# Kernel tuning notes

Measured on AMD Instinct MI355X. Metric: run time of the kernel, lower is better.

## Reference

```python
import jax, jax.numpy as jnp
import numpy as np

N, D, H, C = 100000, 128, 8, 16  # nodes, units=H*C, heads, per-head channels
E = 400000                        # edges per edge set (2 edge sets)
LN_EPS = 1e-3                     # keras LayerNormalization default epsilon


def setup_inputs() -> dict:
    key = jax.random.key(0)
    ks = jax.random.split(key, 16)
    def dense(k, i, o):
        return jax.random.normal(k, (i, o), jnp.float32) / np.float32(np.sqrt(i))
    return dict(
        x=jax.random.normal(ks[0], (N, D), jnp.float32),
        src0=jax.random.randint(ks[1], (E,), 0, N),
        dst0=jax.random.randint(ks[2], (E,), 0, N),
        src1=jax.random.randint(ks[3], (E,), 0, N),
        dst1=jax.random.randint(ks[4], (E,), 0, N),
        Wk=dense(ks[5], D, D), bk=jnp.zeros((D,), jnp.float32),
        Wm=dense(ks[6], D, D), bm=jnp.zeros((D,), jnp.float32),
        Wq=dense(ks[7], D, D), bq=jnp.zeros((D,), jnp.float32),
        Wa=dense(ks[8], D, D), ba=jnp.zeros((D,), jnp.float32),
        Watt0=jax.random.normal(ks[9], (H, C, C), jnp.float32) / np.float32(np.sqrt(C)),
        Wmsg0=jax.random.normal(ks[10], (H, C, C), jnp.float32) / np.float32(np.sqrt(C)),
        Watt1=jax.random.normal(ks[11], (H, C, C), jnp.float32) / np.float32(np.sqrt(C)),
        Wmsg1=jax.random.normal(ks[12], (H, C, C), jnp.float32) / np.float32(np.sqrt(C)),
        prior0=jnp.ones((H,), jnp.float32),
        prior1=jnp.ones((H,), jnp.float32),
        skip=jnp.ones((), jnp.float32),
        gamma=jnp.ones((D,), jnp.float32),
        beta=jnp.zeros((D,), jnp.float32),
    )


def reference(x, src0, dst0, src1, dst1, Wk, bk, Wm, bm, Wq, bq, Wa, ba,
              Watt0, Wmsg0, Watt1, Wmsg1, prior0, prior1, skip, gamma, beta):
    # Node-level projections, split per head: [N, H, C]
    k = (x @ Wk + bk).reshape(N, H, C)
    m = (x @ Wm + bm).reshape(N, H, C)
    q = (x @ Wq + bq).reshape(N, H, C)
    scale = 1.0 / jnp.sqrt(jnp.float32(C))

    def edge_terms(src, dst, Watt, Wmsg, prior):
        # per-edge-type relation projections of gathered sender keys/messages
        ke = jnp.einsum('ehk,hkl->ehl', k[src], Watt)          # [E, H, C]
        score = jnp.einsum('ehl,ehl->eh', ke, q[dst]) * prior * scale  # [E, H]
        msg = jnp.einsum('ehk,hkl->ehl', m[src], Wmsg)          # [E, H, C]
        return score, msg

    s0, m0 = edge_terms(src0, dst0, Watt0, Wmsg0, prior0)
    s1, m1 = edge_terms(src1, dst1, Watt1, Wmsg1, prior1)

    # Joint segment softmax over all incoming edges (both edge sets) per receiver
    scores = jnp.concatenate([s0, s1], axis=0)   # [2E, H]
    msgs = jnp.concatenate([m0, m1], axis=0)     # [2E, H, C]
    recv = jnp.concatenate([dst0, dst1], axis=0)

    smax = jax.ops.segment_max(scores, recv, num_segments=N)   # [N, H]
    ex = jnp.exp(scores - smax[recv])
    denom = jax.ops.segment_sum(ex, recv, num_segments=N)      # [N, H]
    d_e = denom[recv]
    attn = ex / jnp.where(d_e > 0, d_e, 1.0)                   # [2E, H]

    pooled = jax.ops.segment_sum(attn[:, :, None] * msgs, recv,
                                 num_segments=N).reshape(N, D)  # [N, D]

    # aggr(gelu(pooled)); weighted skip; layer norm
    h = jax.nn.gelu(pooled, approximate=False) @ Wa + ba
    alpha = jax.nn.sigmoid(skip)
    out = alpha * h + (1.0 - alpha) * x
    mu = jnp.mean(out, axis=-1, keepdims=True)
    var = jnp.var(out, axis=-1, keepdims=True)
    out = (out - mu) * jax.lax.rsqrt(var + LN_EPS) * gamma + beta
    return out
```

## Files before the change

kernel.cpp:

```cpp
#include <hip/hip_runtime.h>
#include <hip/hip_bf16.h>
#include <math.h>

#define N_NODES 100000
#define DIM 128
#define NH 8
#define NC 16
#define E_EDGES 400000
#define LN_EPS 1e-3f
#define SCAN_B 1024

typedef __attribute__((ext_vector_type(8))) short short8v;
typedef __attribute__((ext_vector_type(4))) float float4v;

__global__ __launch_bounds__(256) void xcast_kernel(
    const float4* __restrict__ x4, __hip_bfloat162* __restrict__ xb2)
{
    int i = blockIdx.x * 256 + threadIdx.x;
    if (i < (N_NODES * DIM) / 4) {
        float4 v = x4[i];
        __hip_bfloat162 a, b;
        a.x = __float2bfloat16(v.x); a.y = __float2bfloat16(v.y);
        b.x = __float2bfloat16(v.z); b.y = __float2bfloat16(v.w);
        xb2[2 * i] = a;
        xb2[2 * i + 1] = b;
    }
}

__global__ __launch_bounds__(128) void fuse_weights(
    const float* __restrict__ Wk, const float* __restrict__ bk,
    const float* __restrict__ Wm, const float* __restrict__ bm,
    const float* __restrict__ Wq, const float* __restrict__ bq,
    const float* __restrict__ Wa, const float* __restrict__ ba,
    const float* __restrict__ Watt0, const float* __restrict__ Wmsg0,
    const float* __restrict__ Watt1, const float* __restrict__ Wmsg1,
    const float* __restrict__ prior0, const float* __restrict__ prior1,
    __hip_bfloat16* __restrict__ Wt, float* __restrict__ bias)
{
    const int c = blockIdx.x;
    const int d = threadIdx.x;
    const int sec = c >> 7, j = c & 127, h = j >> 4, l = j & 15;
    float v, b;
    if (sec == 4)      { v = Wq[d * DIM + j]; b = bq[j]; }
    else if (sec == 5) { v = Wa[d * DIM + j]; b = ba[j]; }
    else {
        const float* W1 = (sec < 2) ? Wk : Wm;
        const float* bs = (sec < 2) ? bk : bm;
        const float* W2 = (sec == 0) ? Watt0 : (sec == 1) ? Watt1
                          : (sec == 2) ? Wmsg0 : Wmsg1;
        float scale = (sec == 0) ? prior0[h] * 0.25f
                    : (sec == 1) ? prior1[h] * 0.25f : 1.f;
        float s = 0.f, sb = 0.f;
        #pragma unroll
        for (int kk = 0; kk < NC; ++kk) {
            float w2 = W2[h * 256 + kk * 16 + l];
            s  = fmaf(W1[d * DIM + h * 16 + kk], w2, s);
            sb = fmaf(bs[h * 16 + kk], w2, sb);
        }
        v = s * scale; b = sb * scale;
    }
    Wt[(size_t)c * DIM + d] = __float2bfloat16(v);
    if (d == 0) bias[c] = b;
}

__global__ __launch_bounds__(256) void proj_mfma(
    const __hip_bfloat16* __restrict__ xb,
    const __hip_bfloat16* __restrict__ Wt,
    const float* __restrict__ bias,
    __hip_bfloat16* __restrict__ kattC,
    __hip_bfloat16* __restrict__ mmsgC,
    float* __restrict__ qout)
{
    const int wave = threadIdx.x >> 6, lane = threadIdx.x & 63;
    const int quad = lane >> 4, mcol = lane & 15;
    const int r0 = blockIdx.x * 32;

    short8v a0[4], a1[4];
    const short* xp0 = (const short*)xb + (size_t)(r0 + mcol) * DIM + quad * 8;
    const short* xp1 = xp0 + 16 * DIM;
    #pragma unroll
    for (int kb = 0; kb < 4; ++kb) {
        a0[kb] = *(const short8v*)(xp0 + kb * 32);
        a1[kb] = *(const short8v*)(xp1 + kb * 32);
    }

    #pragma unroll
    for (int t = 0; t < 10; ++t) {
        const int c0 = wave * 160 + t * 16;
        const short* wp = (const short*)Wt + (size_t)(c0 + mcol) * DIM + quad * 8;
        float4v acc0 = {0.f, 0.f, 0.f, 0.f};
        float4v acc1 = {0.f, 0.f, 0.f, 0.f};
        #pragma unroll
        for (int kb = 0; kb < 4; ++kb) {
            short8v bfr = *(const short8v*)(wp + kb * 32);
            acc0 = __builtin_amdgcn_mfma_f32_16x16x32_bf16(a0[kb], bfr, acc0, 0, 0, 0);
            acc1 = __builtin_amdgcn_mfma_f32_16x16x32_bf16(a1[kb], bfr, acc1, 0, 0, 0);
        }
        const float bcol = bias[c0 + mcol];
        const int sec = c0 >> 7;
        const int cc = (c0 & 127) + mcol;
        const int rb0 = r0 + quad * 4;
        if (sec == 4) {
            #pragma unroll
            for (int g = 0; g < 4; ++g) {
                qout[(size_t)(rb0 + g) * DIM + cc]      = acc0[g] + bcol;
                qout[(size_t)(rb0 + 16 + g) * DIM + cc] = acc1[g] + bcol;
            }
        } else {
            __hip_bfloat16* dst = (sec < 2) ? kattC : mmsgC;
            const size_t off = (sec & 1) ? (size_t)N_NODES * DIM : 0;
            #pragma unroll
            for (int g = 0; g < 4; ++g) {
                dst[off + (size_t)(rb0 + g) * DIM + cc]      = __float2bfloat16(acc0[g] + bcol);
                dst[off + (size_t)(rb0 + 16 + g) * DIM + cc] = __float2bfloat16(acc1[g] + bcol);
            }
        }
    }
}

__global__ __launch_bounds__(256) void hist_kernel(
    const int* __restrict__ dst0, const int* __restrict__ dst1,
    int* __restrict__ counts)
{
    int e = blockIdx.x * 256 + threadIdx.x;
    if (e < E_EDGES) atomicAdd(&counts[dst0[e]], 1);
    int e1 = e - E_EDGES;
    if (e1 >= 0 && e1 < E_EDGES) atomicAdd(&counts[dst1[e1]], 1);
}

__global__ __launch_bounds__(SCAN_B) void scanA_kernel(
    const int* __restrict__ counts, int* __restrict__ row_ptr,
    int* __restrict__ bsum)
{
    __shared__ int buf[2][SCAN_B];
    int i = blockIdx.x * SCAN_B + threadIdx.x;
    int v = (i < N_NODES) ? counts[i] : 0;
    int cur = 0;
    buf[0][threadIdx.x] = v;
    __syncthreads();
    #pragma unroll
    for (int off = 1; off < SCAN_B; off <<= 1) {
        int t = buf[cur][threadIdx.x];
        int add = (threadIdx.x >= off) ? buf[cur][threadIdx.x - off] : 0;
        buf[cur ^ 1][threadIdx.x] = t + add;
        cur ^= 1;
        __syncthreads();
    }
    int inc = buf[cur][threadIdx.x];
    if (i < N_NODES) row_ptr[i] = inc - v;
    if (threadIdx.x == SCAN_B - 1) bsum[blockIdx.x] = inc;
}

__global__ void scanB_kernel(int* __restrict__ bsum, int nblocks)
{
    if (threadIdx.x == 0 && blockIdx.x == 0) {
        int running = 0;
        for (int b = 0; b < nblocks; ++b) {
            int t = bsum[b]; bsum[b] = running; running += t;
        }
    }
}

__global__ __launch_bounds__(SCAN_B) void scanC_kernel(
    int* __restrict__ row_ptr, int* __restrict__ cursor,
    const int* __restrict__ bsum)
{
    int i = blockIdx.x * SCAN_B + threadIdx.x;
    if (i < N_NODES) {
        int r = row_ptr[i] + bsum[blockIdx.x];
        row_ptr[i] = r;
        cursor[i] = r;
    }
}

__global__ __launch_bounds__(256) void scatter_kernel(
    const int* __restrict__ src0, const int* __restrict__ dst0,
    const int* __restrict__ src1, const int* __restrict__ dst1,
    int* __restrict__ cursor, unsigned int* __restrict__ eidx)
{
    int e = blockIdx.x * 256 + threadIdx.x;
    if (e < E_EDGES) {
        int d = dst0[e];
        int pos = atomicAdd(&cursor[d], 1);
        eidx[pos] = (unsigned int)src0[e];
    }
    int e1 = e - E_EDGES;
    if (e1 >= 0 && e1 < E_EDGES) {
        int d = dst1[e1];
        int pos = atomicAdd(&cursor[d], 1);
        eidx[pos] = (unsigned int)(src1[e1] + N_NODES);
    }
}

__global__ __launch_bounds__(256) void agg_kernel(
    const __hip_bfloat162* __restrict__ katt,
    const __hip_bfloat162* __restrict__ mmsg,
    const float2* __restrict__ q2,
    const int* __restrict__ row_ptr, const int* __restrict__ counts,
    const unsigned int* __restrict__ eidx,
    __hip_bfloat162* __restrict__ pooled2)
{
    const int wave = threadIdx.x >> 6, lane = threadIdx.x & 63;
    const int n = blockIdx.x * 4 + wave;
    if (n >= N_NODES) return;
    const int start = row_ptr[n], cnt = counts[n];
    const float2 qq = q2[(size_t)n * 64 + lane];

    float accx = 0.f, accy = 0.f, den = 0.f;
    int i = 0;
    for (; i + 2 <= cnt; i += 2) {
        unsigned int r0 = eidx[start + i];
        unsigned int r1 = eidx[start + i + 1];
        __hip_bfloat162 ka0 = katt[(size_t)r0 * 64 + lane];
        __hip_bfloat162 ka1 = katt[(size_t)r1 * 64 + lane];
        __hip_bfloat162 mg0 = mmsg[(size_t)r0 * 64 + lane];
        __hip_bfloat162 mg1 = mmsg[(size_t)r1 * 64 + lane];
        float p0 = fmaf(__bfloat162float(ka0.x), qq.x,
                        __bfloat162float(ka0.y) * qq.y);
        float p1 = fmaf(__bfloat162float(ka1.x), qq.x,
                        __bfloat162float(ka1.y) * qq.y);
        p0 += __shfl_xor(p0, 1, 64); p0 += __shfl_xor(p0, 2, 64); p0 += __shfl_xor(p0, 4, 64);
        p1 += __shfl_xor(p1, 1, 64); p1 += __shfl_xor(p1, 2, 64); p1 += __shfl_xor(p1, 4, 64);
        float e0 = expf(p0), e1 = expf(p1);
        accx = fmaf(e0, __bfloat162float(mg0.x), accx);
        accy = fmaf(e0, __bfloat162float(mg0.y), accy);
        accx = fmaf(e1, __bfloat162float(mg1.x), accx);
        accy = fmaf(e1, __bfloat162float(mg1.y), accy);
        den += e0 + e1;
    }
    if (i < cnt) {
        unsigned int r0 = eidx[start + i];
        __hip_bfloat162 ka0 = katt[(size_t)r0 * 64 + lane];
        __hip_bfloat162 mg0 = mmsg[(size_t)r0 * 64 + lane];
        float p0 = fmaf(__bfloat162float(ka0.x), qq.x,
                        __bfloat162float(ka0.y) * qq.y);
        p0 += __shfl_xor(p0, 1, 64); p0 += __shfl_xor(p0, 2, 64); p0 += __shfl_xor(p0, 4, 64);
        float e0 = expf(p0);
        accx = fmaf(e0, __bfloat162float(mg0.x), accx);
        accy = fmaf(e0, __bfloat162float(mg0.y), accy);
        den += e0;
    }

    float vx = 0.f, vy = 0.f;
    if (den > 0.f) { vx = accx / den; vy = accy / den; }
    vx = 0.5f * vx * (1.f + erff(vx * 0.70710678118654752f));
    vy = 0.5f * vy * (1.f + erff(vy * 0.70710678118654752f));
    __hip_bfloat162 o; o.x = __float2bfloat16(vx); o.y = __float2bfloat16(vy);
    pooled2[(size_t)n * 64 + lane] = o;
}

__global__ __launch_bounds__(256) void final_mfma(
    const __hip_bfloat16* __restrict__ pooled,
    const __hip_bfloat16* __restrict__ Wt,
    const float* __restrict__ bias,
    const float* __restrict__ x,
    const float* __restrict__ skip, const float* __restrict__ gamma,
    const float* __restrict__ beta, float* __restrict__ out)
{
    __shared__ float hs[32][DIM];
    const int wave = threadIdx.x >> 6, lane = threadIdx.x & 63;
    const int quad = lane >> 4, mcol = lane & 15;
    const int r0 = blockIdx.x * 32;

    short8v a0[4], a1[4];
    const short* pp0 = (const short*)pooled + (size_t)(r0 + mcol) * DIM + quad * 8;
    const short* pp1 = pp0 + 16 * DIM;
    #pragma unroll
    for (int kb = 0; kb < 4; ++kb) {
        a0[kb] = *(const short8v*)(pp0 + kb * 32);
        a1[kb] = *(const short8v*)(pp1 + kb * 32);
    }
    const float alpha = 1.f / (1.f + expf(-skip[0]));

    #pragma unroll
    for (int t = 0; t < 2; ++t) {
        const int c0 = wave * 32 + t * 16;
        const short* wp = (const short*)Wt + (size_t)(640 + c0 + mcol) * DIM + quad * 8;
        float4v acc0 = {0.f, 0.f, 0.f, 0.f};
        float4v acc1 = {0.f, 0.f, 0.f, 0.f};
        #pragma unroll
        for (int kb = 0; kb < 4; ++kb) {
            short8v bfr = *(const short8v*)(wp + kb * 32);
            acc0 = __builtin_amdgcn_mfma_f32_16x16x32_bf16(a0[kb], bfr, acc0, 0, 0, 0);
            acc1 = __builtin_amdgcn_mfma_f32_16x16x32_bf16(a1[kb], bfr, acc1, 0, 0, 0);
        }
        const float bcol = bias[640 + c0 + mcol];
        const int cc = c0 + mcol;
        const int rq = quad * 4;
        #pragma unroll
        for (int g = 0; g < 4; ++g) {
            int rA = rq + g, rB = rq + 16 + g;
            hs[rA][cc] = alpha * (acc0[g] + bcol)
                       + (1.f - alpha) * x[(size_t)(r0 + rA) * DIM + cc];
            hs[rB][cc] = alpha * (acc1[g] + bcol)
                       + (1.f - alpha) * x[(size_t)(r0 + rB) * DIM + cc];
        }
    }
    __syncthreads();

    float gam0 = gamma[lane], gam1 = gamma[lane + 64];
    float bet0 = beta[lane],  bet1 = beta[lane + 64];
    for (int r = wave; r < 32; r += 4) {
        int row = r0 + r;
        float v0 = hs[r][lane], v1 = hs[r][lane + 64];
        float s = v0 + v1, s2 = v0 * v0 + v1 * v1;
        #pragma unroll
        for (int off = 1; off < 64; off <<= 1) {
            s  += __shfl_xor(s,  off, 64);
            s2 += __shfl_xor(s2, off, 64);
        }
        float mu = s * (1.f / 128.f);
        float var = s2 * (1.f / 128.f) - mu * mu;
        float rstd = rsqrtf(var + LN_EPS);
        out[(size_t)row * DIM + lane]      = (v0 - mu) * rstd * gam0 + bet0;
        out[(size_t)row * DIM + lane + 64] = (v1 - mu) * rstd * gam1 + bet1;
    }
}

extern "C" void kernel_launch(void* const* d_in, const int* in_sizes, int n_in,
                              void* d_out, int out_size, void* d_ws, size_t ws_size,
                              hipStream_t stream) {
    const float* x     = (const float*)d_in[0];
    const int*   src0  = (const int*)d_in[1];
    const int*   dst0  = (const int*)d_in[2];
    const int*   src1  = (const int*)d_in[3];
    const int*   dst1  = (const int*)d_in[4];
    const float* Wk    = (const float*)d_in[5];
    const float* bk    = (const float*)d_in[6];
    const float* Wm    = (const float*)d_in[7];
    const float* bm    = (const float*)d_in[8];
    const float* Wq    = (const float*)d_in[9];
    const float* bq    = (const float*)d_in[10];
    const float* Wa    = (const float*)d_in[11];
    const float* ba    = (const float*)d_in[12];
    const float* Watt0 = (const float*)d_in[13];
    const float* Wmsg0 = (const float*)d_in[14];
    const float* Watt1 = (const float*)d_in[15];
    const float* Wmsg1 = (const float*)d_in[16];
    const float* prior0= (const float*)d_in[17];
    const float* prior1= (const float*)d_in[18];
    const float* skip  = (const float*)d_in[19];
    const float* gamma = (const float*)d_in[20];
    const float* beta  = (const float*)d_in[21];
    float* out = (float*)d_out;

    const size_t nd = (size_t)N_NODES * DIM;
    char* wsb = (char*)d_ws;
    __hip_bfloat16* xb    = (__hip_bfloat16*)wsb;  wsb += nd * 2;
    __hip_bfloat16* Wt    = (__hip_bfloat16*)wsb;  wsb += (size_t)768 * DIM * 2;
    float* bias           = (float*)wsb;           wsb += 768 * 4;
    __hip_bfloat16* kattC = (__hip_bfloat16*)wsb;  wsb += 2 * nd * 2;
    __hip_bfloat16* mmsgC = (__hip_bfloat16*)wsb;  wsb += 2 * nd * 2;
    __hip_bfloat16* pooled= (__hip_bfloat16*)wsb;  wsb += nd * 2;
    int* counts  = (int*)wsb;                      wsb += (size_t)N_NODES * 4;
    int* row_ptr = (int*)wsb;                      wsb += (size_t)N_NODES * 4;
    int* cursor  = (int*)wsb;                      wsb += (size_t)N_NODES * 4;
    int* bsum    = (int*)wsb;                      wsb += 128 * 4;
    unsigned int* eidx = (unsigned int*)wsb;
    float* qbuf = out;

    hipMemsetAsync(counts, 0, (size_t)N_NODES * 4, stream);

    const int scan_blocks = (N_NODES + SCAN_B - 1) / SCAN_B;
    const int edge_blocks = (2 * E_EDGES + 255) / 256;

    hist_kernel<<<dim3(edge_blocks), dim3(256), 0, stream>>>(dst0, dst1, counts);
    scanA_kernel<<<dim3(scan_blocks), dim3(SCAN_B), 0, stream>>>(counts, row_ptr, bsum);
    scanB_kernel<<<dim3(1), dim3(64), 0, stream>>>(bsum, scan_blocks);
    scanC_kernel<<<dim3(scan_blocks), dim3(SCAN_B), 0, stream>>>(row_ptr, cursor, bsum);
    scatter_kernel<<<dim3(edge_blocks), dim3(256), 0, stream>>>(
        src0, dst0, src1, dst1, cursor, eidx);

    xcast_kernel<<<dim3((N_NODES * DIM / 4 + 255) / 256), dim3(256), 0, stream>>>(
        (const float4*)x, (__hip_bfloat162*)xb);
    fuse_weights<<<dim3(768), dim3(128), 0, stream>>>(
        Wk, bk, Wm, bm, Wq, bq, Wa, ba,
        Watt0, Wmsg0, Watt1, Wmsg1, prior0, prior1, Wt, bias);
    proj_mfma<<<dim3(N_NODES / 32), dim3(256), 0, stream>>>(
        xb, Wt, bias, kattC, mmsgC, qbuf);

    agg_kernel<<<dim3((N_NODES + 3) / 4), dim3(256), 0, stream>>>(
        (const __hip_bfloat162*)kattC, (const __hip_bfloat162*)mmsgC,
        (const float2*)qbuf, row_ptr, counts, eidx, (__hip_bfloat162*)pooled);

    final_mfma<<<dim3(N_NODES / 32), dim3(256), 0, stream>>>(
        pooled, Wt, bias, x, skip, gamma, beta, out);
}
```

Measured before the change: 430.9 us.

## Fuse x cast into projection, stage outputs in LDS, store q as bf16

Removes the separate fp32-to-bf16 cast kernel by converting x inside the projection kernel. Projection outputs are staged per 128-column section in shared memory and written with coalesced 16-byte stores. q is now stored in bf16 rather than fp32, which halves its write and read traffic but lowers precision. The block-sum scan becomes a parallel shared-memory scan, and the aggregation switches to fast __expf.

```diff
diff --git a/kernel.cpp b/kernel.cpp
--- a/kernel.cpp
+++ b/kernel.cpp
@@ -13,18 +13,9 @@
 typedef __attribute__((ext_vector_type(8))) short short8v;
 typedef __attribute__((ext_vector_type(4))) float float4v;
 
-__global__ __launch_bounds__(256) void xcast_kernel(
-    const float4* __restrict__ x4, __hip_bfloat162* __restrict__ xb2)
-{
-    int i = blockIdx.x * 256 + threadIdx.x;
-    if (i < (N_NODES * DIM) / 4) {
-        float4 v = x4[i];
-        __hip_bfloat162 a, b;
-        a.x = __float2bfloat16(v.x); a.y = __float2bfloat16(v.y);
-        b.x = __float2bfloat16(v.z); b.y = __float2bfloat16(v.w);
-        xb2[2 * i] = a;
-        xb2[2 * i + 1] = b;
-    }
+__device__ __forceinline__ short bf16bits(float v) {
+    __hip_bfloat16 b = __float2bfloat16(v);
+    return *(short*)&b;
 }
 
 __global__ __launch_bounds__(128) void fuse_weights(
@@ -64,57 +55,66 @@
 }
 
 __global__ __launch_bounds__(256) void proj_mfma(
-    const __hip_bfloat16* __restrict__ xb,
+    const float* __restrict__ x,
     const __hip_bfloat16* __restrict__ Wt,
     const float* __restrict__ bias,
     __hip_bfloat16* __restrict__ kattC,
     __hip_bfloat16* __restrict__ mmsgC,
-    float* __restrict__ qout)
-{
+    __hip_bfloat16* __restrict__ qb)
+{
+    __shared__ short tile[32][DIM];
     const int wave = threadIdx.x >> 6, lane = threadIdx.x & 63;
     const int quad = lane >> 4, mcol = lane & 15;
     const int r0 = blockIdx.x * 32;
 
     short8v a0[4], a1[4];
-    const short* xp0 = (const short*)xb + (size_t)(r0 + mcol) * DIM + quad * 8;
-    const short* xp1 = xp0 + 16 * DIM;
+    const float* xr0 = x + (size_t)(r0 + mcol) * DIM + quad * 8;
+    const float* xr1 = xr0 + 16 * DIM;
     #pragma unroll
     for (int kb = 0; kb < 4; ++kb) {
-        a0[kb] = *(const short8v*)(xp0 + kb * 32);
-        a1[kb] = *(const short8v*)(xp1 + kb * 32);
-    }
-
-    #pragma unroll
-    for (int t = 0; t < 10; ++t) {
-        const int c0 = wave * 160 + t * 16;
-        const short* wp = (const short*)Wt + (size_t)(c0 + mcol) * DIM + quad * 8;
-        float4v acc0 = {0.f, 0.f, 0.f, 0.f};
-        float4v acc1 = {0.f, 0.f, 0.f, 0.f};
-        #pragma unroll
-        for (int kb = 0; kb < 4; ++kb) {
-            short8v bfr = *(const short8v*)(wp + kb * 32);
-            acc0 = __builtin_amdgcn_mfma_f32_16x16x32_bf16(a0[kb], bfr, acc0, 0, 0, 0);
-            acc1 = __builtin_amdgcn_mfma_f32_16x16x32_bf16(a1[kb], bfr, acc1, 0, 0, 0);
-        }
-        const float bcol = bias[c0 + mcol];
-        const int sec = c0 >> 7;
-        const int cc = (c0 & 127) + mcol;
-        const int rb0 = r0 + quad * 4;
-        if (sec == 4) {
+        #pragma unroll
+        for (int jj = 0; jj < 8; ++jj) {
+            a0[kb][jj] = bf16bits(xr0[kb * 32 + jj]);
+            a1[kb][jj] = bf16bits(xr1[kb * 32 + jj]);
+        }
+    }
+
+    const int wrow = threadIdx.x >> 3;
+    const int wcol = (threadIdx.x & 7) * 16;
+    #pragma unroll
+    for (int s = 0; s < 5; ++s) {
+        #pragma unroll
+        for (int tp = 0; tp < 2; ++tp) {
+            const int ct = (wave + tp * 4) * 16;
+            const int c0 = s * 128 + ct;
+            const short* wp = (const short*)Wt + (size_t)(c0 + mcol) * DIM + quad * 8;
+            float4v acc0 = {0.f, 0.f, 0.f, 0.f};
+            float4v acc1 = {0.f, 0.f, 0.f, 0.f};
+            #pragma unroll
+            for (int kb = 0; kb < 4; ++kb) {
+                short8v bfr = *(const short8v*)(wp + kb * 32);
+                acc0 = __builtin_amdgcn_mfma_f32_16x16x32_bf16(a0[kb], bfr, acc0, 0, 0, 0);
+                acc1 = __builtin_amdgcn_mfma_f32_16x16x32_bf16(a1[kb], bfr, acc1, 0, 0, 0);
+            }
+            const float bcol = bias[c0 + mcol];
+            const int cc = ct + mcol, rq = quad * 4;
             #pragma unroll
             for (int g = 0; g < 4; ++g) {
-                qout[(size_t)(rb0 + g) * DIM + cc]      = acc0[g] + bcol;
-                qout[(size_t)(rb0 + 16 + g) * DIM + cc] = acc1[g] + bcol;
+                tile[rq + g][cc]      = bf16bits(acc0[g] + bcol);
+                tile[rq + 16 + g][cc] = bf16bits(acc1[g] + bcol);
             }
-        } else {
-            __hip_bfloat16* dst = (sec < 2) ? kattC : mmsgC;
-            const size_t off = (sec & 1) ? (size_t)N_NODES * DIM : 0;
-            #pragma unroll
-            for (int g = 0; g < 4; ++g) {
-                dst[off + (size_t)(rb0 + g) * DIM + cc]      = __float2bfloat16(acc0[g] + bcol);
-                dst[off + (size_t)(rb0 + 16 + g) * DIM + cc] = __float2bfloat16(acc1[g] + bcol);
-            }
-        }
+        }
+        __syncthreads();
+        __hip_bfloat16* dst =
+            (s == 0) ? kattC + (size_t)r0 * DIM :
+            (s == 1) ? kattC + ((size_t)N_NODES + r0) * DIM :
+            (s == 2) ? mmsgC + (size_t)r0 * DIM :
+            (s == 3) ? mmsgC + ((size_t)N_NODES + r0) * DIM :
+                       qb    + (size_t)r0 * DIM;
+        short* dp = (short*)dst + (size_t)wrow * DIM + wcol;
+        *(short8v*)dp       = *(short8v*)&tile[wrow][wcol];
+        *(short8v*)(dp + 8) = *(short8v*)&tile[wrow][wcol + 8];
+        __syncthreads();
     }
 }
 
@@ -151,14 +151,23 @@
     if (threadIdx.x == SCAN_B - 1) bsum[blockIdx.x] = inc;
 }
 
-__global__ void scanB_kernel(int* __restrict__ bsum, int nblocks)
-{
-    if (threadIdx.x == 0 && blockIdx.x == 0) {
-        int running = 0;
-        for (int b = 0; b < nblocks; ++b) {
-            int t = bsum[b]; bsum[b] = running; running += t;
-        }
-    }
+__global__ __launch_bounds__(128) void scanB_kernel(int* __restrict__ bsum, int nblocks)
+{
+    __shared__ int buf[2][128];
+    int t = threadIdx.x;
+    int v = (t < nblocks) ? bsum[t] : 0;
+    buf[0][t] = v;
+    __syncthreads();
+    int cur = 0;
+    #pragma unroll
+    for (int off = 1; off < 128; off <<= 1) {
+        int a = buf[cur][t];
+        if (t >= off) a += buf[cur][t - off];
+        buf[cur ^ 1][t] = a;
+        cur ^= 1;
+        __syncthreads();
+    }
+    if (t < nblocks) bsum[t] = buf[cur][t] - v;
 }
 
 __global__ __launch_bounds__(SCAN_B) void scanC_kernel(
@@ -195,7 +204,7 @@
 __global__ __launch_bounds__(256) void agg_kernel(
     const __hip_bfloat162* __restrict__ katt,
     const __hip_bfloat162* __restrict__ mmsg,
-    const float2* __restrict__ q2,
+    const __hip_bfloat162* __restrict__ qb2,
     const int* __restrict__ row_ptr, const int* __restrict__ counts,
     const unsigned int* __restrict__ eidx,
     __hip_bfloat162* __restrict__ pooled2)
@@ -204,7 +213,8 @@
     const int n = blockIdx.x * 4 + wave;
     if (n >= N_NODES) return;
     const int start = row_ptr[n], cnt = counts[n];
-    const float2 qq = q2[(size_t)n * 64 + lane];
+    __hip_bfloat162 qv = qb2[(size_t)n * 64 + lane];
+    const float qx = __bfloat162float(qv.x), qy = __bfloat162float(qv.y);
 
     float accx = 0.f, accy = 0.f, den = 0.f;
     int i = 0;
@@ -215,13 +225,13 @@
         __hip_bfloat162 ka1 = katt[(size_t)r1 * 64 + lane];
         __hip_bfloat162 mg0 = mmsg[(size_t)r0 * 64 + lane];
         __hip_bfloat162 mg1 = mmsg[(size_t)r1 * 64 + lane];
-        float p0 = fmaf(__bfloat162float(ka0.x), qq.x,
-                        __bfloat162float(ka0.y) * qq.y);
-        float p1 = fmaf(__bfloat162float(ka1.x), qq.x,
-                        __bfloat162float(ka1.y) * qq.y);
+        float p0 = fmaf(__bfloat162float(ka0.x), qx,
+                        __bfloat162float(ka0.y) * qy);
+        float p1 = fmaf(__bfloat162float(ka1.x), qx,
+                        __bfloat162float(ka1.y) * qy);
         p0 += __shfl_xor(p0, 1, 64); p0 += __shfl_xor(p0, 2, 64); p0 += __shfl_xor(p0, 4, 64);
         p1 += __shfl_xor(p1, 1, 64); p1 += __shfl_xor(p1, 2, 64); p1 += __shfl_xor(p1, 4, 64);
-        float e0 = expf(p0), e1 = expf(p1);
+        float e0 = __expf(p0), e1 = __expf(p1);
         accx = fmaf(e0, __bfloat162float(mg0.x), accx);
         accy = fmaf(e0, __bfloat162float(mg0.y), accy);
         accx = fmaf(e1, __bfloat162float(mg1.x), accx);
@@ -232,10 +242,10 @@
         unsigned int r0 = eidx[start + i];
         __hip_bfloat162 ka0 = katt[(size_t)r0 * 64 + lane];
         __hip_bfloat162 mg0 = mmsg[(size_t)r0 * 64 + lane];
-        float p0 = fmaf(__bfloat162float(ka0.x), qq.x,
-                        __bfloat162float(ka0.y) * qq.y);
+        float p0 = fmaf(__bfloat162float(ka0.x), qx,
+                        __bfloat162float(ka0.y) * qy);
         p0 += __shfl_xor(p0, 1, 64); p0 += __shfl_xor(p0, 2, 64); p0 += __shfl_xor(p0, 4, 64);
-        float e0 = expf(p0);
+        float e0 = __expf(p0);
         accx = fmaf(e0, __bfloat162float(mg0.x), accx);
         accy = fmaf(e0, __bfloat162float(mg0.y), accy);
         den += e0;
@@ -346,18 +356,17 @@
 
     const size_t nd = (size_t)N_NODES * DIM;
     char* wsb = (char*)d_ws;
-    __hip_bfloat16* xb    = (__hip_bfloat16*)wsb;  wsb += nd * 2;
     __hip_bfloat16* Wt    = (__hip_bfloat16*)wsb;  wsb += (size_t)768 * DIM * 2;
     float* bias           = (float*)wsb;           wsb += 768 * 4;
     __hip_bfloat16* kattC = (__hip_bfloat16*)wsb;  wsb += 2 * nd * 2;
     __hip_bfloat16* mmsgC = (__hip_bfloat16*)wsb;  wsb += 2 * nd * 2;
+    __hip_bfloat16* qb    = (__hip_bfloat16*)wsb;  wsb += nd * 2;
     __hip_bfloat16* pooled= (__hip_bfloat16*)wsb;  wsb += nd * 2;
     int* counts  = (int*)wsb;                      wsb += (size_t)N_NODES * 4;
     int* row_ptr = (int*)wsb;                      wsb += (size_t)N_NODES * 4;
     int* cursor  = (int*)wsb;                      wsb += (size_t)N_NODES * 4;
     int* bsum    = (int*)wsb;                      wsb += 128 * 4;
     unsigned int* eidx = (unsigned int*)wsb;
-    float* qbuf = out;
 
     hipMemsetAsync(counts, 0, (size_t)N_NODES * 4, stream);
 
@@ -366,22 +375,21 @@
 
     hist_kernel<<<dim3(edge_blocks), dim3(256), 0, stream>>>(dst0, dst1, counts);
     scanA_kernel<<<dim3(scan_blocks), dim3(SCAN_B), 0, stream>>>(counts, row_ptr, bsum);
-    scanB_kernel<<<dim3(1), dim3(64), 0, stream>>>(bsum, scan_blocks);
+    scanB_kernel<<<dim3(1), dim3(128), 0, stream>>>(bsum, scan_blocks);
     scanC_kernel<<<dim3(scan_blocks), dim3(SCAN_B), 0, stream>>>(row_ptr, cursor, bsum);
     scatter_kernel<<<dim3(edge_blocks), dim3(256), 0, stream>>>(
         src0, dst0, src1, dst1, cursor, eidx);
 
-    xcast_kernel<<<dim3((N_NODES * DIM / 4 + 255) / 256), dim3(256), 0, stream>>>(
-        (const float4*)x, (__hip_bfloat162*)xb);
     fuse_weights<<<dim3(768), dim3(128), 0, stream>>>(
         Wk, bk, Wm, bm, Wq, bq, Wa, ba,
         Watt0, Wmsg0, Watt1, Wmsg1, prior0, prior1, Wt, bias);
     proj_mfma<<<dim3(N_NODES / 32), dim3(256), 0, stream>>>(
-        xb, Wt, bias, kattC, mmsgC, qbuf);
+        x, Wt, bias, kattC, mmsgC, qb);
 
     agg_kernel<<<dim3((N_NODES + 3) / 4), dim3(256), 0, stream>>>(
         (const __hip_bfloat162*)kattC, (const __hip_bfloat162*)mmsgC,
-        (const float2*)qbuf, row_ptr, counts, eidx, (__hip_bfloat162*)pooled);
+        (const __hip_bfloat162*)qb, row_ptr, counts, eidx,
+        (__hip_bfloat162*)pooled);
 
     final_mfma<<<dim3(N_NODES / 32), dim3(256), 0, stream>>>(
         pooled, Wt, bias, x, skip, gamma, beta, out);
```

Result: faster. 415.3 us (-3.6%).
